# Kernel optimization log

Measured on AMD Instinct MI355X. Metric: run time of the kernel, lower is better.

Reference implementation:

```python
import jax, jax.numpy as jnp
import numpy as np

# Haar (db1) filters after the index reversals done in create_wavelet_filter.
_S = np.float32(1.0 / np.sqrt(2.0))
_LO = np.array([_S, _S], np.float32)
_HI = np.array([_S, -_S], np.float32)
# dec[k, i, j]; band order: LL, (hi rows)*lo, lo*(hi cols), HH -> matches torch stack order
_DEC = np.stack([np.outer(_LO, _LO), np.outer(_HI, _LO), np.outer(_LO, _HI), np.outer(_HI, _HI)], 0)
_REC = _DEC  # identical for Haar


def dwt(x):
    # non-overlapping 2x2 stride-2 depthwise conv == blocked einsum
    b, c, h, w = x.shape
    xr = x.reshape(b, c, h // 2, 2, w // 2, 2)
    return jnp.einsum('bcipjq,kpq->bckij', xr, jnp.asarray(_DEC))  # [b,c,4,h/2,w/2]


def idwt(x):
    # stride-2 kernel-2 transposed depthwise conv == blocked einsum
    b, c, _, h, w = x.shape
    y = jnp.einsum('bckij,kpq->bcipjq', x, jnp.asarray(_REC))
    return y.reshape(b, c, 2 * h, 2 * w)


def dwconv3(x, w, bias=None):
    # depthwise 3x3 'same' conv; w: [C,1,3,3]
    c = x.shape[1]
    y = jax.lax.conv_general_dilated(x, w, (1, 1), 'SAME', feature_group_count=c,
                                     dimension_numbers=('NCHW', 'OIHW', 'NCHW'))
    if bias is not None:
        y = y + bias[None, :, None, None]
    return y


def setup_inputs() -> dict:
    key = jax.random.key(0)
    ks = jax.random.split(key, 8)
    B, C, H, W = 16, 64, 256, 256
    inp = {
        'x': jax.random.normal(ks[0], (B, C, H, W), jnp.float32),
        'base_w': jax.random.normal(ks[1], (C, 1, 3, 3), jnp.float32) * 0.1,
        'base_b': jax.random.normal(ks[2], (C,), jnp.float32) * 0.01,
        'base_scale': jnp.ones((1, C, 1, 1), jnp.float32),
        'ww0': jax.random.normal(ks[3], (4 * C, 1, 3, 3), jnp.float32) * 0.1,
        'ww1': jax.random.normal(ks[4], (4 * C, 1, 3, 3), jnp.float32) * 0.1,
        'ww2': jax.random.normal(ks[5], (4 * C, 1, 3, 3), jnp.float32) * 0.1,
        'ws0': jnp.full((1, 4 * C, 1, 1), 0.1, jnp.float32),
        'ws1': jnp.full((1, 4 * C, 1, 1), 0.1, jnp.float32),
        'ws2': jnp.full((1, 4 * C, 1, 1), 0.1, jnp.float32),
        'gamma': jnp.ones((C,), jnp.float32),
        'beta': jnp.zeros((C,), jnp.float32),
    }
    return inp


def reference(x, base_w, base_b, base_scale, ww0, ww1, ww2, ws0, ws1, ws2, gamma, beta):
    wws = [ww0, ww1, ww2]
    wss = [ws0, ws1, ws2]
    levels = 3
    lls, hs = [], []
    cur = x
    # --- WTConv2d: recursive wavelet pyramid (H,W divisible by 2**levels, no odd-pad) ---
    for i in range(levels):
        cx = dwt(cur)                # [b,c,4,h/2,w/2]
        cur = cx[:, :, 0]            # LL feeds next level
        b_, c_, _, h_, w_ = cx.shape
        t = cx.reshape(b_, c_ * 4, h_, w_)
        t = dwconv3(t, wws[i]) * wss[i]   # depthwise conv (no bias) + learned scale
        t = t.reshape(b_, c_, 4, h_, w_)
        lls.append(t[:, :, 0])
        hs.append(t[:, :, 1:4])
    nxt = jnp.zeros_like(lls[-1])
    for i in range(levels - 1, -1, -1):
        ll = lls[i] + nxt
        cx = jnp.concatenate([ll[:, :, None], hs[i]], axis=2)
        nxt = idwt(cx)
    # base depthwise conv path
    y = dwconv3(x, base_w, base_b) * base_scale + nxt
    # --- BatchNorm2d (training-mode batch stats, eps=1e-5) + ReLU ---
    mean = y.mean(axis=(0, 2, 3), keepdims=True)
    var = ((y - mean) ** 2).mean(axis=(0, 2, 3), keepdims=True)
    y = (y - mean) * jax.lax.rsqrt(var + 1e-5)
    y = y * gamma[None, :, None, None] + beta[None, :, None, None]
    return jax.nn.relu(y)
```

## Files before the change

kernel.cpp:

```cpp
#include <hip/hip_runtime.h>
#include <hip/hip_bf16.h>

#define NB 16
#define NC 64

static __device__ __forceinline__ unsigned short f2bfr(float f) {
    union { float f; unsigned u; } cv; cv.f = f;
    unsigned r = cv.u + 0x7fffu + ((cv.u >> 16) & 1u);
    return (unsigned short)(r >> 16);
}
static __device__ __forceinline__ float bfr2f(unsigned short h) {
    union { unsigned u; float f; } cv; cv.u = ((unsigned)h) << 16;
    return cv.f;
}
static __device__ __forceinline__ unsigned pack2bf(float lo, float hi) {
    return ((unsigned)f2bfr(lo)) | (((unsigned)f2bfr(hi)) << 16);
}

template <int H>
static __device__ __forceinline__ void stage_tile(
    const float* __restrict__ src, size_t ibase, int sTop, int sLeft,
    float (*sIn)[76], int tid)
{
#pragma unroll
    for (int i = 0; i < 5; ++i) {
        int idx = i * 256 + tid;
        if (idx < 68 * 16) {
            int r = idx >> 4, c4 = (idx & 15) << 2;
            int gy = sTop + r, gx = sLeft + c4;
            float4 v = make_float4(0.f, 0.f, 0.f, 0.f);
            if ((unsigned)gy < (unsigned)H && (unsigned)gx < (unsigned)H)
                v = *(const float4*)(src + ibase + (size_t)gy * H + gx);
            *(float4*)(&sIn[r][c4]) = v;
        }
    }
    if (tid < 136) {
        int r = tid >> 1, c4 = 64 + ((tid & 1) << 2);
        int gy = sTop + r, gx = sLeft + c4;
        float4 v = make_float4(0.f, 0.f, 0.f, 0.f);
        if ((unsigned)gy < (unsigned)H && (unsigned)gx < (unsigned)H)
            v = *(const float4*)(src + ibase + (size_t)gy * H + gx);
        *(float4*)(&sIn[r][c4]) = v;
    }
}

__global__ __launch_bounds__(256) void ll_kernel(
    const float* __restrict__ in, float* __restrict__ ll)
{
    int t = blockIdx.x * 256 + threadIdx.x;
    int jp  = t & 63;
    int i   = (t >> 6) & 127;
    int img = t >> 13;
    size_t ib = (size_t)img * 65536;
    float4 a = *(const float4*)(in + ib + (size_t)(2 * i) * 256 + 4 * jp);
    float4 b = *(const float4*)(in + ib + (size_t)(2 * i + 1) * 256 + 4 * jp);
    float2 o;
    o.x = 0.5f * (a.x + a.y + b.x + b.y);
    o.y = 0.5f * (a.z + a.w + b.z + b.w);
    *(float2*)(ll + (size_t)img * 16384 + (size_t)i * 128 + 2 * jp) = o;
}

template <int H>
__global__ __launch_bounds__(256) void dwt_conv_kernel(
    const float* __restrict__ in, const float* __restrict__ ww,
    const float* __restrict__ wsc, unsigned short* __restrict__ t_out,
    float* __restrict__ curn)
{
    constexpr int H2 = H / 2;
    constexpr int TX = H2 / 32;
    const int tile = blockIdx.x;
    const int c = blockIdx.y, b = blockIdx.z;
    const int ty = tile / TX, tx = tile % TX;
    const int oy0 = ty * 32, ox0 = tx * 32;
    const int tid = threadIdx.x;
    const int qi = 2 * (tid >> 4), qj = 2 * (tid & 15);

    __shared__ float sIn[68][76];

    float w[4][9], sc[4];
#pragma unroll
    for (int k = 0; k < 4; ++k) {
#pragma unroll
        for (int i = 0; i < 9; ++i) w[k][i] = ww[(c * 4 + k) * 9 + i];
        sc[k] = 0.5f * wsc[c * 4 + k];
    }

    const size_t ibase = (size_t)(b * NC + c) * H * H;
    stage_tile<H>(in, ibase, 2 * oy0 - 2, 2 * ox0 - 4, sIn, tid);
    __syncthreads();

    float kk[4][4];
#pragma unroll
    for (int i = 0; i < 4; ++i)
#pragma unroll
        for (int j = 0; j < 4; ++j) kk[i][j] = 0.f;
    float llc[4];

    const int pr0 = 2 * qi, pc0 = 2 * qj + 2;
#pragma unroll
    for (int rp = 0; rp < 4; ++rp) {
        float xa[8], xb[8];
#pragma unroll
        for (int n = 0; n < 4; ++n) {
            float2 va = *(const float2*)&sIn[pr0 + 2 * rp][pc0 + 2 * n];
            float2 vb = *(const float2*)&sIn[pr0 + 2 * rp + 1][pc0 + 2 * n];
            xa[2 * n] = va.x; xa[2 * n + 1] = va.y;
            xb[2 * n] = vb.x; xb[2 * n + 1] = vb.y;
        }
        float D0[4], D1[4], D2[4], D3[4];
#pragma unroll
        for (int n = 0; n < 4; ++n) {
            float a = xa[2 * n], e = xa[2 * n + 1];
            float f = xb[2 * n], g = xb[2 * n + 1];
            float s0 = a + e, s1 = f + g, d0 = a - e, d1 = f - g;
            D0[n] = s0 + s1; D1[n] = s0 - s1;
            D2[n] = d0 + d1; D3[n] = d0 - d1;
        }
#pragma unroll
        for (int mi = 0; mi < 2; ++mi) {
            const int r = rp - mi;
            if (r >= 0 && r <= 2) {
#pragma unroll
                for (int mj = 0; mj < 2; ++mj) {
                    const int m = 2 * mi + mj;
#pragma unroll
                    for (int s = 0; s < 3; ++s) {
                        kk[0][m] = fmaf(w[0][3 * r + s], D0[mj + s], kk[0][m]);
                        kk[1][m] = fmaf(w[1][3 * r + s], D1[mj + s], kk[1][m]);
                        kk[2][m] = fmaf(w[2][3 * r + s], D2[mj + s], kk[2][m]);
                        kk[3][m] = fmaf(w[3][3 * r + s], D3[mj + s], kk[3][m]);
                    }
                }
                if (r == 1) {
                    llc[2 * mi + 0] = 0.5f * D0[1];
                    llc[2 * mi + 1] = 0.5f * D0[2];
                }
            }
        }
    }

    const size_t tbase = (size_t)(b * NC + c) * 4 * H2 * H2;
    const size_t o00 = (size_t)(oy0 + qi) * H2 + (ox0 + qj);
#pragma unroll
    for (int band = 0; band < 4; ++band) {
        size_t bo = tbase + (size_t)band * H2 * H2 + o00;
#pragma unroll
        for (int mi = 0; mi < 2; ++mi)
            *(unsigned*)(t_out + bo + (size_t)mi * H2) =
                pack2bf(kk[band][2 * mi] * sc[band], kk[band][2 * mi + 1] * sc[band]);
    }
    if (curn) {
        const size_t cbase = (size_t)(b * NC + c) * H2 * H2 + o00;
        *(float2*)(curn + cbase)      = make_float2(llc[0], llc[1]);
        *(float2*)(curn + cbase + H2) = make_float2(llc[2], llc[3]);
    }
}

__global__ __launch_bounds__(256) void idwt_fuse_kernel(
    const unsigned short* __restrict__ t1, const unsigned short* __restrict__ t2,
    unsigned short* __restrict__ nxt1)
{
    int idx = blockIdx.x * 256 + threadIdx.x;
    int j = idx & 63, i = (idx >> 6) & 63, img = idx >> 12;
    size_t t2b = (size_t)img * 4096 + (size_t)(i >> 1) * 32 + (j >> 1);
    float m0 = bfr2f(t2[t2b]);
    float m1 = bfr2f(t2[t2b + 1024]);
    float m2 = bfr2f(t2[t2b + 2048]);
    float m3 = bfr2f(t2[t2b + 3072]);
    float a1 = (i & 1) ? -m1 : m1;
    float a2 = (j & 1) ? -m2 : m2;
    float a3 = ((i ^ j) & 1) ? -m3 : m3;
    float nxt2v = 0.5f * (m0 + a1 + a2 + a3);
    size_t t1b = (size_t)img * 16384 + (size_t)i * 64 + j;
    float k0 = bfr2f(t1[t1b]) + nxt2v;
    float k1 = bfr2f(t1[t1b + 4096]);
    float k2 = bfr2f(t1[t1b + 8192]);
    float k3 = bfr2f(t1[t1b + 12288]);
    size_t ob = (size_t)img * 16384 + (size_t)(2 * i) * 128 + 2 * j;
    *(unsigned*)(nxt1 + ob)       = pack2bf(0.5f * (k0 + k1 + k2 + k3),
                                            0.5f * (k0 + k1 - k2 - k3));
    *(unsigned*)(nxt1 + ob + 128) = pack2bf(0.5f * (k0 - k1 + k2 - k3),
                                            0.5f * (k0 - k1 - k2 + k3));
}

__global__ __launch_bounds__(256) void final_fuse_kernel(
    const float* __restrict__ x, const unsigned short* __restrict__ nxt1,
    const float* __restrict__ bw, const float* __restrict__ bb,
    const float* __restrict__ bs, const float* __restrict__ ww0,
    const float* __restrict__ ws0,
    unsigned short* __restrict__ ybf, float2* __restrict__ partials)
{
    const int tile = blockIdx.x, c = blockIdx.y, b = blockIdx.z;
    const int ty = tile >> 2, tx = tile & 3;
    const int oy0 = ty * 64, ox0 = tx * 64;
    const int hy0 = ty * 32, hx0 = tx * 32;
    const int tid = threadIdx.x;

    __shared__ float sIn[68][76];
    __shared__ float rS[256], rQ[256];

    float w[4][9], sc[4], wb[9];
#pragma unroll
    for (int k = 0; k < 4; ++k) {
#pragma unroll
        for (int i = 0; i < 9; ++i) w[k][i] = ww0[(c * 4 + k) * 9 + i];
        sc[k] = 0.25f * ws0[c * 4 + k];
    }
#pragma unroll
    for (int i = 0; i < 9; ++i) wb[i] = bw[c * 9 + i];
    const float scale = bs[c];
    const float bsc = bb[c] * scale;

    const size_t xb = (size_t)(b * NC + c) * 65536;
    stage_tile<256>(x, xb, oy0 - 2, ox0 - 4, sIn, tid);
    __syncthreads();

    const size_t n1b = (size_t)(b * NC + c) * 16384;
    const int qj = tid & 31;
    const int qi0 = tid >> 5;
    float lsum = 0.f, lss = 0.f;
#pragma unroll
    for (int it = 0; it < 4; ++it) {
        int qi = qi0 + 8 * it;
        float P[6][6];
#pragma unroll
        for (int r = 0; r < 6; ++r) {
            const float2* rp = (const float2*)&sIn[2 * qi + r][2 * qj + 2];
            float2 p0 = rp[0], p1 = rp[1], p2 = rp[2];
            P[r][0] = p0.x; P[r][1] = p0.y; P[r][2] = p1.x;
            P[r][3] = p1.y; P[r][4] = p2.x; P[r][5] = p2.y;
        }
        float kk0 = 0.f, kk1 = 0.f, kk2 = 0.f, kk3 = 0.f;
#pragma unroll
        for (int r = 0; r < 3; ++r)
#pragma unroll
            for (int s = 0; s < 3; ++s) {
                float a = P[2*r][2*s],   e = P[2*r][2*s+1];
                float f = P[2*r+1][2*s], g = P[2*r+1][2*s+1];
                float s0 = a + e, s1 = f + g, d0 = a - e, d1 = f - g;
                kk0 += w[0][3*r+s] * (s0 + s1);
                kk1 += w[1][3*r+s] * (s0 - s1);
                kk2 += w[2][3*r+s] * (d0 + d1);
                kk3 += w[3][3*r+s] * (d0 - d1);
            }
        kk0 = kk0 * sc[0] + 0.5f * bfr2f(nxt1[n1b + (size_t)(hy0 + qi) * 128 + (hx0 + qj)]);
        kk1 *= sc[1];
        kk2 *= sc[2];
        kk3 *= sc[3];
        float vv[2][2];
        vv[0][0] = kk0 + kk1 + kk2 + kk3;
        vv[0][1] = kk0 + kk1 - kk2 - kk3;
        vv[1][0] = kk0 - kk1 + kk2 - kk3;
        vv[1][1] = kk0 - kk1 - kk2 + kk3;
        int yl = 2 * qi, xl = 2 * qj;
#pragma unroll
        for (int p = 0; p < 2; ++p) {
            unsigned pack = 0;
#pragma unroll
            for (int q = 0; q < 2; ++q) {
                float acc = 0.f;
#pragma unroll
                for (int r = 0; r < 3; ++r)
#pragma unroll
                    for (int s = 0; s < 3; ++s)
                        acc += P[p + r + 1][q + s + 1] * wb[3 * r + s];
                float val = fmaf(acc, scale, bsc) + vv[p][q];
                lsum += val;
                lss = fmaf(val, val, lss);
                pack |= ((unsigned)f2bfr(val)) << (16 * q);
            }
            *(unsigned*)(ybf + xb + (size_t)(oy0 + yl + p) * 256 + (ox0 + xl)) = pack;
        }
    }
    rS[tid] = lsum;
    rQ[tid] = lss;
    __syncthreads();
    for (int off = 128; off > 0; off >>= 1) {
        if (tid < off) { rS[tid] += rS[tid + off]; rQ[tid] += rQ[tid + off]; }
        __syncthreads();
    }
    if (tid == 0)
        partials[c * 256 + b * 16 + tile] = make_float2(rS[0], rQ[0]);
}

__global__ __launch_bounds__(256) void stats_kernel(
    const float2* __restrict__ partials, const float* __restrict__ gamma,
    const float* __restrict__ beta, float2* __restrict__ ab)
{
    const int c = blockIdx.x;
    const int tid = threadIdx.x;
    __shared__ float s1[256], s2[256];
    float2 p = partials[c * 256 + tid];
    s1[tid] = p.x;
    s2[tid] = p.y;
    __syncthreads();
    for (int off = 128; off > 0; off >>= 1) {
        if (tid < off) { s1[tid] += s1[tid + off]; s2[tid] += s2[tid + off]; }
        __syncthreads();
    }
    if (tid == 0) {
        const float N = (float)NB * 65536.0f;
        float mean = s1[0] / N;
        float var = s2[0] / N - mean * mean;
        float inv = rsqrtf(var + 1e-5f);
        float a = gamma[c] * inv;
        ab[c] = make_float2(a, beta[c] - mean * a);
    }
}

__global__ __launch_bounds__(256) void norm_out_kernel(
    const unsigned short* __restrict__ ybf, const float2* __restrict__ ab,
    float* __restrict__ out)
{
    const long total8 = (long)NB * NC * 65536 / 8;
    const long stride = (long)gridDim.x * 256;
    for (long i = blockIdx.x * 256L + threadIdx.x; i < total8; i += stride) {
        long e = i * 8;
        int c = (int)((e >> 16) & (NC - 1));
        float2 s = ab[c];
        uint4 v = *(const uint4*)(ybf + e);
        float4 o0, o1;
        o0.x = fmaxf(fmaf(bfr2f((unsigned short)(v.x & 0xffff)), s.x, s.y), 0.f);
        o0.y = fmaxf(fmaf(bfr2f((unsigned short)(v.x >> 16)),    s.x, s.y), 0.f);
        o0.z = fmaxf(fmaf(bfr2f((unsigned short)(v.y & 0xffff)), s.x, s.y), 0.f);
        o0.w = fmaxf(fmaf(bfr2f((unsigned short)(v.y >> 16)),    s.x, s.y), 0.f);
        o1.x = fmaxf(fmaf(bfr2f((unsigned short)(v.z & 0xffff)), s.x, s.y), 0.f);
        o1.y = fmaxf(fmaf(bfr2f((unsigned short)(v.z >> 16)),    s.x, s.y), 0.f);
        o1.z = fmaxf(fmaf(bfr2f((unsigned short)(v.w & 0xffff)), s.x, s.y), 0.f);
        o1.w = fmaxf(fmaf(bfr2f((unsigned short)(v.w >> 16)),    s.x, s.y), 0.f);
        *(float4*)(out + e) = o0;
        *(float4*)(out + e + 4) = o1;
    }
}

extern "C" void kernel_launch(void* const* d_in, const int* in_sizes, int n_in,
                              void* d_out, int out_size, void* d_ws, size_t ws_size,
                              hipStream_t stream)
{
    const float* x    = (const float*)d_in[0];
    const float* bw   = (const float*)d_in[1];
    const float* bb   = (const float*)d_in[2];
    const float* bs   = (const float*)d_in[3];
    const float* ww0  = (const float*)d_in[4];
    const float* ww1  = (const float*)d_in[5];
    const float* ww2  = (const float*)d_in[6];
    const float* ws0  = (const float*)d_in[7];
    const float* ws1  = (const float*)d_in[8];
    const float* ws2  = (const float*)d_in[9];
    const float* gamma = (const float*)d_in[10];
    const float* beta  = (const float*)d_in[11];

    char* w = (char*)d_ws;
    unsigned short* ybf  = (unsigned short*)(w);
    float*          cur1 = (float*)(w);
    unsigned short* t1   = (unsigned short*)(w + 134217728);
    float*          cur2 = (float*)(w + 167772160);
    unsigned short* t2   = (unsigned short*)(w + 184549376);
    unsigned short* nxt1 = (unsigned short*)(w + 192937984);
    float2*         partials = (float2*)(w + 226492416);
    float2*         ab       = (float2*)(w + 226623488);

    ll_kernel<<<dim3(NB * NC * 128 * 64 / 256), 256, 0, stream>>>(x, cur1);
    dwt_conv_kernel<128><<<dim3(4, NC, NB), 256, 0, stream>>>(cur1, ww1, ws1, t1, cur2);
    dwt_conv_kernel<64><<<dim3(1, NC, NB), 256, 0, stream>>>(cur2, ww2, ws2, t2, nullptr);
    idwt_fuse_kernel<<<dim3(NB * NC * 4096 / 256), 256, 0, stream>>>(t1, t2, nxt1);
    final_fuse_kernel<<<dim3(16, NC, NB), 256, 0, stream>>>(x, nxt1, bw, bb, bs, ww0, ws0, ybf, partials);
    stats_kernel<<<dim3(64), 256, 0, stream>>>(partials, gamma, beta, ab);
    norm_out_kernel<<<dim3(2048), 256, 0, stream>>>(ybf, ab, (float*)d_out);
}
```

Baseline: 347.0 us.

## Fuse LL computation into level-1 DWT conv, restructure final fuse kernel

```diff
diff --git a/kernel.cpp b/kernel.cpp
--- a/kernel.cpp
+++ b/kernel.cpp
@@ -4,17 +4,14 @@
 #define NB 16
 #define NC 64
 
-static __device__ __forceinline__ unsigned short f2bfr(float f) {
-    union { float f; unsigned u; } cv; cv.f = f;
-    unsigned r = cv.u + 0x7fffu + ((cv.u >> 16) & 1u);
-    return (unsigned short)(r >> 16);
-}
 static __device__ __forceinline__ float bfr2f(unsigned short h) {
     union { unsigned u; float f; } cv; cv.u = ((unsigned)h) << 16;
     return cv.f;
 }
-static __device__ __forceinline__ unsigned pack2bf(float lo, float hi) {
-    return ((unsigned)f2bfr(lo)) | (((unsigned)f2bfr(hi)) << 16);
+static __device__ __forceinline__ unsigned cvt_pk_bf16(float lo, float hi) {
+    unsigned r;
+    asm("v_cvt_pk_bf16_f32 %0, %1, %2" : "=v"(r) : "v"(lo), "v"(hi));
+    return r;
 }
 
 template <int H>
@@ -44,38 +41,13 @@
     }
 }
 
-__global__ __launch_bounds__(256) void ll_kernel(
-    const float* __restrict__ in, float* __restrict__ ll)
-{
-    int t = blockIdx.x * 256 + threadIdx.x;
-    int jp  = t & 63;
-    int i   = (t >> 6) & 127;
-    int img = t >> 13;
-    size_t ib = (size_t)img * 65536;
-    float4 a = *(const float4*)(in + ib + (size_t)(2 * i) * 256 + 4 * jp);
-    float4 b = *(const float4*)(in + ib + (size_t)(2 * i + 1) * 256 + 4 * jp);
-    float2 o;
-    o.x = 0.5f * (a.x + a.y + b.x + b.y);
-    o.y = 0.5f * (a.z + a.w + b.z + b.w);
-    *(float2*)(ll + (size_t)img * 16384 + (size_t)i * 128 + 2 * jp) = o;
-}
-
-template <int H>
-__global__ __launch_bounds__(256) void dwt_conv_kernel(
-    const float* __restrict__ in, const float* __restrict__ ww,
+template <int H2>
+static __device__ __forceinline__ void dwt_conv_body(
+    const float (*sIn)[76], const float* __restrict__ ww,
     const float* __restrict__ wsc, unsigned short* __restrict__ t_out,
-    float* __restrict__ curn)
-{
-    constexpr int H2 = H / 2;
-    constexpr int TX = H2 / 32;
-    const int tile = blockIdx.x;
-    const int c = blockIdx.y, b = blockIdx.z;
-    const int ty = tile / TX, tx = tile % TX;
-    const int oy0 = ty * 32, ox0 = tx * 32;
-    const int tid = threadIdx.x;
+    float* __restrict__ curn, int c, int b, int oy0, int ox0, int tid)
+{
     const int qi = 2 * (tid >> 4), qj = 2 * (tid & 15);
-
-    __shared__ float sIn[68][76];
 
     float w[4][9], sc[4];
 #pragma unroll
@@ -84,10 +56,6 @@
         for (int i = 0; i < 9; ++i) w[k][i] = ww[(c * 4 + k) * 9 + i];
         sc[k] = 0.5f * wsc[c * 4 + k];
     }
-
-    const size_t ibase = (size_t)(b * NC + c) * H * H;
-    stage_tile<H>(in, ibase, 2 * oy0 - 2, 2 * ox0 - 4, sIn, tid);
-    __syncthreads();
 
     float kk[4][4];
 #pragma unroll
@@ -147,13 +115,60 @@
 #pragma unroll
         for (int mi = 0; mi < 2; ++mi)
             *(unsigned*)(t_out + bo + (size_t)mi * H2) =
-                pack2bf(kk[band][2 * mi] * sc[band], kk[band][2 * mi + 1] * sc[band]);
+                cvt_pk_bf16(kk[band][2 * mi] * sc[band], kk[band][2 * mi + 1] * sc[band]);
     }
     if (curn) {
         const size_t cbase = (size_t)(b * NC + c) * H2 * H2 + o00;
         *(float2*)(curn + cbase)      = make_float2(llc[0], llc[1]);
         *(float2*)(curn + cbase + H2) = make_float2(llc[2], llc[3]);
     }
+}
+
+__global__ __launch_bounds__(256) void dwt_conv_from_x_kernel(
+    const float* __restrict__ x, const float* __restrict__ ww,
+    const float* __restrict__ wsc, unsigned short* __restrict__ t_out,
+    float* __restrict__ curn)
+{
+    const int tile = blockIdx.x;
+    const int c = blockIdx.y, b = blockIdx.z;
+    const int ty = tile >> 1, tx = tile & 1;
+    const int oy0 = ty * 32, ox0 = tx * 32;
+    const int tid = threadIdx.x;
+
+    __shared__ float sLL[68][76];
+
+    const size_t xbase = (size_t)(b * NC + c) * 65536;
+    const int gy0 = 4 * oy0 - 4;
+    const int gx0 = 4 * ox0 - 8;
+    for (int u = tid; u < 68 * 36; u += 256) {
+        int r = u / 36, cp = u - r * 36;
+        int gy = gy0 + 2 * r, gx = gx0 + 4 * cp;
+        float4 va = make_float4(0.f, 0.f, 0.f, 0.f);
+        float4 vb = va;
+        if ((unsigned)gy < 256u && (unsigned)gx < 256u) {
+            va = *(const float4*)(x + xbase + (size_t)gy * 256 + gx);
+            vb = *(const float4*)(x + xbase + (size_t)(gy + 1) * 256 + gx);
+        }
+        *(float2*)(&sLL[r][2 * cp]) =
+            make_float2(0.5f * (va.x + va.y + vb.x + vb.y),
+                        0.5f * (va.z + va.w + vb.z + vb.w));
+    }
+    __syncthreads();
+
+    dwt_conv_body<64>(sLL, ww, wsc, t_out, curn, c, b, oy0, ox0, tid);
+}
+
+__global__ __launch_bounds__(256) void dwt_conv_kernel64(
+    const float* __restrict__ in, const float* __restrict__ ww,
+    const float* __restrict__ wsc, unsigned short* __restrict__ t_out)
+{
+    const int c = blockIdx.y, b = blockIdx.z;
+    const int tid = threadIdx.x;
+    __shared__ float sIn[68][76];
+    const size_t ibase = (size_t)(b * NC + c) * 64 * 64;
+    stage_tile<64>(in, ibase, -2, -4, sIn, tid);
+    __syncthreads();
+    dwt_conv_body<32>(sIn, ww, wsc, t_out, nullptr, c, b, 0, 0, tid);
 }
 
 __global__ __launch_bounds__(256) void idwt_fuse_kernel(
@@ -177,10 +192,10 @@
     float k2 = bfr2f(t1[t1b + 8192]);
     float k3 = bfr2f(t1[t1b + 12288]);
     size_t ob = (size_t)img * 16384 + (size_t)(2 * i) * 128 + 2 * j;
-    *(unsigned*)(nxt1 + ob)       = pack2bf(0.5f * (k0 + k1 + k2 + k3),
-                                            0.5f * (k0 + k1 - k2 - k3));
-    *(unsigned*)(nxt1 + ob + 128) = pack2bf(0.5f * (k0 - k1 + k2 - k3),
-                                            0.5f * (k0 - k1 - k2 + k3));
+    *(unsigned*)(nxt1 + ob)       = cvt_pk_bf16(0.5f * (k0 + k1 + k2 + k3),
+                                                0.5f * (k0 + k1 - k2 - k3));
+    *(unsigned*)(nxt1 + ob + 128) = cvt_pk_bf16(0.5f * (k0 - k1 + k2 - k3),
+                                                0.5f * (k0 - k1 - k2 + k3));
 }
 
 __global__ __launch_bounds__(256) void final_fuse_kernel(
@@ -195,9 +210,11 @@
     const int oy0 = ty * 64, ox0 = tx * 64;
     const int hy0 = ty * 32, hx0 = tx * 32;
     const int tid = threadIdx.x;
+    const int qj = tid & 31;
+    const int pr = tid >> 5;
 
     __shared__ float sIn[68][76];
-    __shared__ float rS[256], rQ[256];
+    __shared__ float2 sW4[4];
 
     float w[4][9], sc[4], wb[9];
 #pragma unroll
@@ -216,71 +233,119 @@
     __syncthreads();
 
     const size_t n1b = (size_t)(b * NC + c) * 16384;
-    const int qj = tid & 31;
-    const int qi0 = tid >> 5;
     float lsum = 0.f, lss = 0.f;
-#pragma unroll
-    for (int it = 0; it < 4; ++it) {
-        int qi = qi0 + 8 * it;
-        float P[6][6];
-#pragma unroll
-        for (int r = 0; r < 6; ++r) {
-            const float2* rp = (const float2*)&sIn[2 * qi + r][2 * qj + 2];
-            float2 p0 = rp[0], p1 = rp[1], p2 = rp[2];
-            P[r][0] = p0.x; P[r][1] = p0.y; P[r][2] = p1.x;
-            P[r][3] = p1.y; P[r][4] = p2.x; P[r][5] = p2.y;
-        }
-        float kk0 = 0.f, kk1 = 0.f, kk2 = 0.f, kk3 = 0.f;
-#pragma unroll
-        for (int r = 0; r < 3; ++r)
-#pragma unroll
-            for (int s = 0; s < 3; ++s) {
-                float a = P[2*r][2*s],   e = P[2*r][2*s+1];
-                float f = P[2*r+1][2*s], g = P[2*r+1][2*s+1];
+
+#pragma unroll
+    for (int pass = 0; pass < 2; ++pass) {
+        const int pair = pr + 8 * pass;
+        const int h0 = 2 * pair;
+        const int prow0 = 4 * pair;
+        const int pc0 = 2 * qj + 2;
+
+        float kkA[4], kkB[4];
+#pragma unroll
+        for (int k = 0; k < 4; ++k) { kkA[k] = 0.f; kkB[k] = 0.f; }
+        float acc[4][2];
+#pragma unroll
+        for (int p = 0; p < 4; ++p) { acc[p][0] = 0.f; acc[p][1] = 0.f; }
+
+#pragma unroll
+        for (int rp = 0; rp < 4; ++rp) {
+            float xa[6], xv[6];
+#pragma unroll
+            for (int n = 0; n < 3; ++n) {
+                float2 va = *(const float2*)&sIn[prow0 + 2 * rp][pc0 + 2 * n];
+                float2 vb = *(const float2*)&sIn[prow0 + 2 * rp + 1][pc0 + 2 * n];
+                xa[2 * n] = va.x; xa[2 * n + 1] = va.y;
+                xv[2 * n] = vb.x; xv[2 * n + 1] = vb.y;
+            }
+            float D0[3], D1[3], D2[3], D3[3];
+#pragma unroll
+            for (int n = 0; n < 3; ++n) {
+                float a = xa[2 * n], e = xa[2 * n + 1];
+                float f = xv[2 * n], g = xv[2 * n + 1];
                 float s0 = a + e, s1 = f + g, d0 = a - e, d1 = f - g;
-                kk0 += w[0][3*r+s] * (s0 + s1);
-                kk1 += w[1][3*r+s] * (s0 - s1);
-                kk2 += w[2][3*r+s] * (d0 + d1);
-                kk3 += w[3][3*r+s] * (d0 - d1);
-            }
-        kk0 = kk0 * sc[0] + 0.5f * bfr2f(nxt1[n1b + (size_t)(hy0 + qi) * 128 + (hx0 + qj)]);
-        kk1 *= sc[1];
-        kk2 *= sc[2];
-        kk3 *= sc[3];
-        float vv[2][2];
-        vv[0][0] = kk0 + kk1 + kk2 + kk3;
-        vv[0][1] = kk0 + kk1 - kk2 - kk3;
-        vv[1][0] = kk0 - kk1 + kk2 - kk3;
-        vv[1][1] = kk0 - kk1 - kk2 + kk3;
-        int yl = 2 * qi, xl = 2 * qj;
-#pragma unroll
-        for (int p = 0; p < 2; ++p) {
-            unsigned pack = 0;
-#pragma unroll
-            for (int q = 0; q < 2; ++q) {
-                float acc = 0.f;
-#pragma unroll
-                for (int r = 0; r < 3; ++r)
-#pragma unroll
-                    for (int s = 0; s < 3; ++s)
-                        acc += P[p + r + 1][q + s + 1] * wb[3 * r + s];
-                float val = fmaf(acc, scale, bsc) + vv[p][q];
-                lsum += val;
-                lss = fmaf(val, val, lss);
-                pack |= ((unsigned)f2bfr(val)) << (16 * q);
-            }
-            *(unsigned*)(ybf + xb + (size_t)(oy0 + yl + p) * 256 + (ox0 + xl)) = pack;
-        }
-    }
-    rS[tid] = lsum;
-    rQ[tid] = lss;
+                D0[n] = s0 + s1; D1[n] = s0 - s1;
+                D2[n] = d0 + d1; D3[n] = d0 - d1;
+            }
+            if (rp <= 2) {
+#pragma unroll
+                for (int s = 0; s < 3; ++s) {
+                    kkA[0] = fmaf(w[0][3 * rp + s], D0[s], kkA[0]);
+                    kkA[1] = fmaf(w[1][3 * rp + s], D1[s], kkA[1]);
+                    kkA[2] = fmaf(w[2][3 * rp + s], D2[s], kkA[2]);
+                    kkA[3] = fmaf(w[3][3 * rp + s], D3[s], kkA[3]);
+                }
+            }
+            if (rp >= 1) {
+                const int r = rp - 1;
+#pragma unroll
+                for (int s = 0; s < 3; ++s) {
+                    kkB[0] = fmaf(w[0][3 * r + s], D0[s], kkB[0]);
+                    kkB[1] = fmaf(w[1][3 * r + s], D1[s], kkB[1]);
+                    kkB[2] = fmaf(w[2][3 * r + s], D2[s], kkB[2]);
+                    kkB[3] = fmaf(w[3][3 * r + s], D3[s], kkB[3]);
+                }
+            }
+#pragma unroll
+            for (int py = 0; py < 4; ++py) {
+                const int rra = 2 * rp - py - 1;
+                if (rra >= 0 && rra <= 2) {
+#pragma unroll
+                    for (int u = 0; u < 2; ++u)
+                        acc[py][u] = fmaf(xa[u + 1], wb[3 * rra],
+                                     fmaf(xa[u + 2], wb[3 * rra + 1],
+                                     fmaf(xa[u + 3], wb[3 * rra + 2], acc[py][u])));
+                }
+                const int rrb = 2 * rp - py;
+                if (rrb >= 0 && rrb <= 2) {
+#pragma unroll
+                    for (int u = 0; u < 2; ++u)
+                        acc[py][u] = fmaf(xv[u + 1], wb[3 * rrb],
+                                     fmaf(xv[u + 2], wb[3 * rrb + 1],
+                                     fmaf(xv[u + 3], wb[3 * rrb + 2], acc[py][u])));
+                }
+            }
+        }
+
+        const float n1A = bfr2f(nxt1[n1b + (size_t)(hy0 + h0) * 128 + (hx0 + qj)]);
+        const float n1B = bfr2f(nxt1[n1b + (size_t)(hy0 + h0 + 1) * 128 + (hx0 + qj)]);
+        const size_t ybase = xb + (size_t)(oy0 + 4 * pair) * 256 + (ox0 + 2 * qj);
+#pragma unroll
+        for (int quad = 0; quad < 2; ++quad) {
+            const float* kk = quad ? kkB : kkA;
+            float c0 = fmaf(kk[0], sc[0], 0.5f * (quad ? n1B : n1A));
+            float c1 = kk[1] * sc[1];
+            float c2 = kk[2] * sc[2];
+            float c3 = kk[3] * sc[3];
+            float vv00 = c0 + c1 + c2 + c3;
+            float vv01 = c0 + c1 - c2 - c3;
+            float vv10 = c0 - c1 + c2 - c3;
+            float vv11 = c0 - c1 - c2 + c3;
+            float v00 = fmaf(acc[2 * quad][0],     scale, bsc) + vv00;
+            float v01 = fmaf(acc[2 * quad][1],     scale, bsc) + vv01;
+            float v10 = fmaf(acc[2 * quad + 1][0], scale, bsc) + vv10;
+            float v11 = fmaf(acc[2 * quad + 1][1], scale, bsc) + vv11;
+            lsum += v00 + v01 + v10 + v11;
+            lss = fmaf(v00, v00, lss); lss = fmaf(v01, v01, lss);
+            lss = fmaf(v10, v10, lss); lss = fmaf(v11, v11, lss);
+            *(unsigned*)(ybf + ybase + (size_t)(2 * quad) * 256)     = cvt_pk_bf16(v00, v01);
+            *(unsigned*)(ybf + ybase + (size_t)(2 * quad + 1) * 256) = cvt_pk_bf16(v10, v11);
+        }
+    }
+
+#pragma unroll
+    for (int off = 32; off > 0; off >>= 1) {
+        lsum += __shfl_xor(lsum, off);
+        lss  += __shfl_xor(lss, off);
+    }
+    if ((tid & 63) == 0) sW4[tid >> 6] = make_float2(lsum, lss);
     __syncthreads();
-    for (int off = 128; off > 0; off >>= 1) {
-        if (tid < off) { rS[tid] += rS[tid + off]; rQ[tid] += rQ[tid + off]; }
-        __syncthreads();
-    }
-    if (tid == 0)
-        partials[c * 256 + b * 16 + tile] = make_float2(rS[0], rQ[0]);
+    if (tid == 0) {
+        float s = sW4[0].x + sW4[1].x + sW4[2].x + sW4[3].x;
+        float q = sW4[0].y + sW4[1].y + sW4[2].y + sW4[3].y;
+        partials[c * 256 + b * 16 + tile] = make_float2(s, q);
+    }
 }
 
 __global__ __launch_bounds__(256) void stats_kernel(
@@ -352,7 +417,6 @@
 
     char* w = (char*)d_ws;
     unsigned short* ybf  = (unsigned short*)(w);
-    float*          cur1 = (float*)(w);
     unsigned short* t1   = (unsigned short*)(w + 134217728);
     float*          cur2 = (float*)(w + 167772160);
     unsigned short* t2   = (unsigned short*)(w + 184549376);
@@ -360,9 +424,8 @@
     float2*         partials = (float2*)(w + 226492416);
     float2*         ab       = (float2*)(w + 226623488);
 
-    ll_kernel<<<dim3(NB * NC * 128 * 64 / 256), 256, 0, stream>>>(x, cur1);
-    dwt_conv_kernel<128><<<dim3(4, NC, NB), 256, 0, stream>>>(cur1, ww1, ws1, t1, cur2);
-    dwt_conv_kernel<64><<<dim3(1, NC, NB), 256, 0, stream>>>(cur2, ww2, ws2, t2, nullptr);
+    dwt_conv_from_x_kernel<<<dim3(4, NC, NB), 256, 0, stream>>>(x, ww1, ws1, t1, cur2);
+    dwt_conv_kernel64<<<dim3(1, NC, NB), 256, 0, stream>>>(cur2, ww2, ws2, t2);
     idwt_fuse_kernel<<<dim3(NB * NC * 4096 / 256), 256, 0, stream>>>(t1, t2, nxt1);
     final_fuse_kernel<<<dim3(16, NC, NB), 256, 0, stream>>>(x, nxt1, bw, bb, bs, ww0, ws0, ybf, partials);
     stats_kernel<<<dim3(64), 256, 0, stream>>>(partials, gamma, beta, ab);
```

New measurement: 316.7 us. 1.1x faster.
